# Performance work log

Measured on AMD Instinct MI355X. Metric: run time of the kernel, lower is better.

## Reference

```python
import jax, jax.numpy as jnp
import numpy as np

L, C, FC, H, W, K = 6, 256, 1024, 4, 10, 3
B, T = 4, 1024
KC = C // H


def _get_rel_emb(emb, length):
    # emb: [1, 2W+1, KC] -> [1, 2*length-1, KC]
    pad_len = max(length - (W + 1), 0)
    start = max(W + 1 - length, 0)
    if pad_len > 0:
        emb = jnp.pad(emb, ((0, 0), (pad_len, pad_len), (0, 0)))
    return emb[:, start:start + 2 * length - 1]


def _rel_to_abs(x):
    # [b,h,l,2l-1] -> [b,h,l,l] via pad/reshape shift trick
    b, h, l, _ = x.shape
    x = jnp.pad(x, ((0, 0), (0, 0), (0, 0), (0, 1)))
    x = x.reshape(b, h, l * 2 * l)
    x = jnp.pad(x, ((0, 0), (0, 0), (0, l - 1)))
    return x.reshape(b, h, l + 1, 2 * l - 1)[:, :, :l, l - 1:]


def _abs_to_rel(x):
    # [b,h,l,l] -> [b,h,l,2l-1]
    b, h, l, _ = x.shape
    x = jnp.pad(x, ((0, 0), (0, 0), (0, 0), (0, l - 1)))
    x = x.reshape(b, h, l * l + l * (l - 1))
    x = jnp.pad(x, ((0, 0), (0, 0), (l, 0)))
    return x.reshape(b, h, l, 2 * l)[:, :, :, 1:]


def _ln(x, g, b, eps=1e-5):
    # channel-wise LayerNorm over dim 1 of [B,C,T]
    m = x.mean(axis=1, keepdims=True)
    v = ((x - m) ** 2).mean(axis=1, keepdims=True)
    return (x - m) * jax.lax.rsqrt(v + eps) * g[None, :, None] + b[None, :, None]


def _conv1(x, w, b):
    # pointwise Conv1d: x [B,Cin,T], w [Cout,Cin]
    return jnp.einsum('oc,bct->bot', w, x) + b[None, :, None]


def _convk(x, w, b):
    # Conv1d: x [B,Cin,Tpad], w [Cout,Cin,K], VALID
    y = jax.lax.conv_general_dilated(x, w, (1,), 'VALID', dimension_numbers=('NCH', 'OIH', 'NCH'))
    return y + b[None, :, None]


def _attn(x, mask, wq, bq, wk, bk, wv, bv, wo, bo, erk, erv):
    b, d, t = x.shape
    q = _conv1(x, wq, bq)
    k = _conv1(x, wk, bk)
    v = _conv1(x, wv, bv)
    def split(z):
        return z.reshape(b, H, KC, t).transpose(0, 1, 3, 2)  # [b,h,t,kc]
    qh = split(q) / np.sqrt(KC).astype(np.float32)
    kh = split(k)
    vh = split(v)
    scores = jnp.einsum('bhld,bhmd->bhlm', qh, kh)
    rel_k = _get_rel_emb(erk, t)[0]  # [2t-1, kc]
    scores = scores + _rel_to_abs(jnp.einsum('bhld,md->bhlm', qh, rel_k))
    scores = jnp.where(mask == 0, jnp.float32(-1e4), scores)
    p = jax.nn.softmax(scores, axis=-1)
    out = jnp.einsum('bhlm,bhmd->bhld', p, vh)
    rel_v = _get_rel_emb(erv, t)[0]
    out = out + jnp.einsum('bhlm,md->bhld', _abs_to_rel(p), rel_v)
    out = out.transpose(0, 1, 3, 2).reshape(b, d, t)
    return _conv1(out, wo, bo)


def _ffn(x, mask, w1, b1, w2, b2):
    pl, pr = (K - 1) // 2, K // 2
    def pad_t(z):
        return jnp.pad(z * mask, ((0, 0), (0, 0), (pl, pr)))
    h = jax.nn.relu(_convk(pad_t(x), w1, b1))
    return _convk(pad_t(h), w2, b2) * mask


def setup_inputs() -> dict:
    key = jax.random.key(0)
    ks = jax.random.split(key, 12)
    s = 0.05
    return {
        'x': jax.random.normal(ks[0], (B, C, T), jnp.float32),
        'x_mask': jnp.ones((B, 1, T), jnp.float32),
        'wq': s * jax.random.normal(ks[1], (L, C, C), jnp.float32),
        'bq': jnp.zeros((L, C), jnp.float32),
        'wk': s * jax.random.normal(ks[2], (L, C, C), jnp.float32),
        'bk': jnp.zeros((L, C), jnp.float32),
        'wv': s * jax.random.normal(ks[3], (L, C, C), jnp.float32),
        'bv': jnp.zeros((L, C), jnp.float32),
        'wo': s * jax.random.normal(ks[4], (L, C, C), jnp.float32),
        'bo': jnp.zeros((L, C), jnp.float32),
        'erk': (KC ** -0.5) * jax.random.normal(ks[5], (L, 1, 2 * W + 1, KC), jnp.float32),
        'erv': (KC ** -0.5) * jax.random.normal(ks[6], (L, 1, 2 * W + 1, KC), jnp.float32),
        'ln1_g': jnp.ones((L, C), jnp.float32),
        'ln1_b': jnp.zeros((L, C), jnp.float32),
        'ffn_w1': s * jax.random.normal(ks[7], (L, FC, C, K), jnp.float32),
        'ffn_b1': jnp.zeros((L, FC), jnp.float32),
        'ffn_w2': s * jax.random.normal(ks[8], (L, C, FC, K), jnp.float32),
        'ffn_b2': jnp.zeros((L, C), jnp.float32),
        'ln2_g': jnp.ones((L, C), jnp.float32),
        'ln2_b': jnp.zeros((L, C), jnp.float32),
    }


def reference(x, x_mask, wq, bq, wk, bk, wv, bv, wo, bo, erk, erv, ln1_g, ln1_b, ffn_w1, ffn_b1, ffn_w2, ffn_b2, ln2_g, ln2_b):
    attn_mask = x_mask[:, :, None, :] * x_mask[:, :, :, None]  # [B,1,T,T]
    x = x * x_mask
    for i in range(L):
        y = _attn(x, attn_mask, wq[i], bq[i], wk[i], bk[i], wv[i], bv[i], wo[i], bo[i], erk[i], erv[i])
        x = _ln(x + y, ln1_g[i], ln1_b[i])
        y = _ffn(x, x_mask, ffn_w1[i], ffn_b1[i], ffn_w2[i], ffn_b2[i])
        x = _ln(x + y, ln2_g[i], ln2_b[i])
    return x * x_mask
```

## Files before the change

### kernel.cpp

```cpp
#include <hip/hip_runtime.h>


#define Lz 6
#define Cz 256
#define FCz 1024
#define Hz 4
#define Wz 10
#define Bz 4
#define Tz 1024
#define KCz 64
#define NR 21
#define TS 1032
#define PADF 4
#define PROWS 1026
#define MFIX 8.0f

typedef unsigned short u16;
typedef unsigned int u32;
typedef __attribute__((ext_vector_type(8))) short bf8v;
typedef __attribute__((ext_vector_type(4))) float f4v;

#define MFMA(a, b, c) __builtin_amdgcn_mfma_f32_16x16x32_bf16(a, b, c, 0, 0, 0)

__device__ inline void bf_split(float v, u16& hi, u16& lo) {
  unsigned u = __float_as_uint(v);
  unsigned hr = (u + 0x7FFFu + ((u >> 16) & 1u)) >> 16;
  float rem = v - __uint_as_float(hr << 16);
  unsigned u2 = __float_as_uint(rem);
  unsigned lr = (u2 + 0x7FFFu + ((u2 >> 16) & 1u)) >> 16;
  hi = (u16)hr;
  lo = (u16)lr;
}

__device__ inline u16 bf_rne(float v) {
  u32 u = __float_as_uint(v);
  return (u16)((u + 0x7FFFu + ((u >> 16) & 1u)) >> 16);
}

__global__ __launch_bounds__(256) void mask_in(const float* __restrict__ x,
                                               const float* __restrict__ m,
                                               float* __restrict__ xp) {
  int id = blockIdx.x * 256 + threadIdx.x;
  if (id < Bz * Cz * Tz) {
    int t = id & (Tz - 1), row = id >> 10, b = id >> 18;
    xp[(size_t)row * TS + PADF + t] = x[id] * m[b * Tz + t];
  }
}

__global__ __launch_bounds__(256) void mask_out(const float* __restrict__ xp,
                                                const float* __restrict__ m,
                                                float* __restrict__ out) {
  int id = blockIdx.x * 256 + threadIdx.x;
  if (id < Bz * Cz * Tz) {
    int t = id & (Tz - 1), row = id >> 10, b = id >> 18;
    out[id] = xp[(size_t)row * TS + PADF + t] * m[b * Tz + t];
  }
}

__global__ __launch_bounds__(256) void zero_halo(u16* hi, u16* lo, int Cd) {
  int id = blockIdx.x * 256 + threadIdx.x;
  if (id >= Bz * 2 * Cd) return;
  int c = id % Cd, rb = id / Cd, b = rb >> 1, s = rb & 1;
  size_t a = ((size_t)b * PROWS + (s ? (PROWS - 1) : 0)) * Cd + c;
  hi[a] = 0;
  lo[a] = 0;
}

__global__ __launch_bounds__(256) void tpack(const float* __restrict__ src,
                                             const float* __restrict__ mask,
                                             u16* __restrict__ dhi,
                                             u16* __restrict__ dlo, int Cd) {
  __shared__ float L[64 * 68];
  const int tid = threadIdx.x;
  const int t0 = blockIdx.x * 64, c0 = blockIdx.y * 64, b = blockIdx.z;
  const float* sb = src + (size_t)b * Cd * TS + PADF;
#pragma unroll
  for (int i = 0; i < 16; i++) {
    int id = tid + 256 * i;
    int cc = id >> 6, tt = id & 63;
    L[cc * 68 + tt] = sb[(size_t)(c0 + cc) * TS + t0 + tt];
  }
  __syncthreads();
  const int tt = tid >> 2, p = tid & 3;
  float mv = mask[(size_t)b * Tz + t0 + tt];
  u16 hs[16], ls[16];
#pragma unroll
  for (int j = 0; j < 16; j++) {
    float v = L[(p * 16 + j) * 68 + tt] * mv;
    bf_split(v, hs[j], ls[j]);
  }
  size_t da = ((size_t)b * PROWS + t0 + tt + 1) * Cd + c0 + p * 16;
  *(uint4*)&dhi[da] = *(uint4*)&hs[0];
  *(uint4*)&dhi[da + 8] = *(uint4*)&hs[8];
  *(uint4*)&dlo[da] = *(uint4*)&ls[0];
  *(uint4*)&dlo[da + 8] = *(uint4*)&ls[8];
}

__global__ __launch_bounds__(256) void pack_all(
    const float* __restrict__ wq, const float* __restrict__ wk,
    const float* __restrict__ wv, const float* __restrict__ wo_,
    const float* __restrict__ bq, const float* __restrict__ bk,
    const float* __restrict__ bv, const float* __restrict__ bo,
    const float* __restrict__ erk, const float* __restrict__ erv,
    const float* __restrict__ fw1, const float* __restrict__ fw2,
    u16* __restrict__ qwH, float* __restrict__ pb, u16* __restrict__ ekH,
    u16* __restrict__ evH, u16* __restrict__ w1H, u16* __restrict__ w1L,
    u16* __restrict__ w2H, u16* __restrict__ w2L) {
  const int blk = blockIdx.x, tid = threadIdx.x;
  if (blk < 1024) {
    int id = blk * 256 + tid;
    int o = id >> 8, c = id & 255;
    int sel = o >> 8;
    const float* w = sel == 0 ? wq : (sel == 1 ? wk : (sel == 2 ? wv : wo_));
    qwH[id] = bf_rne(w[((size_t)(o & 255) << 8) + c]);
    if (id < 1024) {
      int s2 = id >> 8;
      const float* bs = s2 == 0 ? bq : (s2 == 1 ? bk : (s2 == 2 ? bv : bo));
      pb[id] = bs[id & 255];
    }
  } else if (blk < 1040) {
    int id = (blk - 1024) * 256 + tid;
    if (id < 2048) {
      int rr = id >> 6, d = id & 63;
      ekH[id] = bf_rne((rr < NR) ? erk[rr * KCz + d] : 0.f);
    } else {
      int id2 = id - 2048;
      int d = id2 >> 5, rr = id2 & 31;
      evH[id2] = bf_rne((rr < NR) ? erv[rr * KCz + d] : 0.f);
    }
  } else if (blk < 4112) {
    int id = (blk - 1040) * 256 + tid;
    int c = id % Cz;
    int rest = id / Cz;
    int o = rest % FCz, tap = rest / FCz;
    float v = fw1[((size_t)o * Cz + c) * 3 + tap];
    bf_split(v, w1H[id], w1L[id]);
  } else {
    int id = (blk - 4112) * 256 + tid;
    int c = id % FCz;
    int rest = id / FCz;
    int o = rest % Cz, tap = rest / Cz;
    float v = fw2[((size_t)o * FCz + c) * 3 + tap];
    bf_split(v, w2H[id], w2L[id]);
  }
}

template <int EPI>
__global__ __launch_bounds__(256) void mfma_gemm2(
    const u16* __restrict__ Ah, const u16* __restrict__ Bh,
    const u16* __restrict__ Bl, const float* __restrict__ bias,
    const float* __restrict__ mask, float* __restrict__ out,
    float* __restrict__ out2, u16* __restrict__ pqh, u16* __restrict__ pql,
    u16* __restrict__ pkh, u16* __restrict__ pvh, int M, int Kc, int m_base) {
  __shared__ __align__(16) char smraw[17408];
  u16* Ash = (u16*)smraw;
  u16* Bsh = Ash + 2560;
  u16* Bsl = Bsh + 2560;
  const int tid = threadIdx.x;
  const int lane = tid & 63, wid = tid >> 6;
  const int wm = wid & 1, wn = wid >> 1;
  const int r = lane & 15, qd = lane >> 4;
  const int t0 = blockIdx.x * 64;
  const int b = blockIdx.z;
  const int srow = tid >> 2, sseg = (tid & 3) * 8;

  int m0, kc0, kcN;
  float* outp = out;
  if constexpr (EPI == 3) {
    m0 = m_base + (blockIdx.y >> 1) * 64;
    kc0 = (blockIdx.y & 1) * (Kc / 2);
    kcN = Kc / 2;
    outp = (blockIdx.y & 1) ? out2 : out;
  } else {
    m0 = blockIdx.y * 64 + m_base;
    kc0 = 0;
    kcN = Kc;
  }

  f4v acc[2][2];
#pragma unroll
  for (int i = 0; i < 2; i++)
#pragma unroll
    for (int j = 0; j < 2; j++) acc[i][j] = (f4v)(0.f);

  const size_t arow = (size_t)(m0 + srow) * Kc + kc0;
  const size_t brow = ((size_t)b * PROWS + t0 + 1 + srow) * Kc + kc0;
  for (int kc = 0; kc < kcN; kc += 32) {
    *(uint4*)&Ash[srow * 40 + sseg] = *(const uint4*)&Ah[arow + kc + sseg];
    *(uint4*)&Bsh[srow * 40 + sseg] = *(const uint4*)&Bh[brow + kc + sseg];
    *(uint4*)&Bsl[srow * 40 + sseg] = *(const uint4*)&Bl[brow + kc + sseg];
    __syncthreads();
    bf8v ah[2], bh2[2], bl2[2];
#pragma unroll
    for (int f = 0; f < 2; f++) {
      int ar = (wm * 32 + f * 16 + r) * 40 + qd * 8;
      int br = (wn * 32 + f * 16 + r) * 40 + qd * 8;
      ah[f] = *(bf8v*)&Ash[ar];
      bh2[f] = *(bf8v*)&Bsh[br];
      bl2[f] = *(bf8v*)&Bsl[br];
    }
#pragma unroll
    for (int mf = 0; mf < 2; mf++)
#pragma unroll
      for (int nf = 0; nf < 2; nf++) {
        acc[mf][nf] = MFMA(ah[mf], bh2[nf], acc[mf][nf]);
        acc[mf][nf] = MFMA(ah[mf], bl2[nf], acc[mf][nf]);
      }
    __syncthreads();
  }

  float* Ds = (float*)smraw;
  if constexpr (EPI == 0) {
    const int sel = m0 >> 8;
    const int h = (m0 >> 6) & 3;
    const int bhI = b * Hz + h;
    if (sel < 2) {
#pragma unroll
      for (int mf = 0; mf < 2; mf++)
#pragma unroll
        for (int nf = 0; nf < 2; nf++) {
          int nl = wn * 32 + nf * 16 + r;
          int ml = wm * 32 + mf * 16 + qd * 4;
          *(f4v*)&Ds[nl * 68 + ml] = acc[mf][nf];
        }
      __syncthreads();
      const int row = tid >> 2, p = tid & 3;
      size_t da = ((size_t)bhI * Tz + t0 + row) * KCz + p * 16;
      if (sel == 0) {
        u16 hs[16], ls[16];
#pragma unroll
        for (int jj = 0; jj < 4; jj++) {
          float4 dv = *(float4*)&Ds[row * 68 + p * 16 + jj * 4];
          float4 bb = *(const float4*)&bias[m0 + p * 16 + jj * 4];
          float vv[4] = {(dv.x + bb.x) * 0.125f, (dv.y + bb.y) * 0.125f,
                         (dv.z + bb.z) * 0.125f, (dv.w + bb.w) * 0.125f};
#pragma unroll
          for (int e = 0; e < 4; e++)
            bf_split(vv[e], hs[jj * 4 + e], ls[jj * 4 + e]);
        }
        *(uint4*)&pqh[da] = *(uint4*)&hs[0];
        *(uint4*)&pqh[da + 8] = *(uint4*)&hs[8];
        *(uint4*)&pql[da] = *(uint4*)&ls[0];
        *(uint4*)&pql[da + 8] = *(uint4*)&ls[8];
      } else {
        u16 hs[16];
#pragma unroll
        for (int jj = 0; jj < 4; jj++) {
          float4 dv = *(float4*)&Ds[row * 68 + p * 16 + jj * 4];
          float4 bb = *(const float4*)&bias[m0 + p * 16 + jj * 4];
          hs[jj * 4 + 0] = bf_rne(dv.x + bb.x);
          hs[jj * 4 + 1] = bf_rne(dv.y + bb.y);
          hs[jj * 4 + 2] = bf_rne(dv.z + bb.z);
          hs[jj * 4 + 3] = bf_rne(dv.w + bb.w);
        }
        *(uint4*)&pkh[da] = *(uint4*)&hs[0];
        *(uint4*)&pkh[da + 8] = *(uint4*)&hs[8];
      }
    } else {
#pragma unroll
      for (int mf = 0; mf < 2; mf++)
#pragma unroll
        for (int nf = 0; nf < 2; nf++) {
          int ml = wm * 32 + mf * 16 + qd * 4;
          int nl = wn * 32 + nf * 16 + r;
#pragma unroll
          for (int e = 0; e < 4; e++) Ds[(ml + e) * 68 + nl] = acc[mf][nf][e];
        }
      __syncthreads();
      const int row = tid >> 2, p = tid & 3;
      const float bb = bias[m0 + row];
      u16 hs[16];
#pragma unroll
      for (int jj = 0; jj < 16; jj++)
        hs[jj] = bf_rne(Ds[row * 68 + p * 16 + jj] + bb);
      size_t da = ((size_t)bhI * KCz + row) * Tz + t0 + p * 16;
      *(uint4*)&pvh[da] = *(uint4*)&hs[0];
      *(uint4*)&pvh[da + 8] = *(uint4*)&hs[8];
    }
  } else {
#pragma unroll
    for (int mf = 0; mf < 2; mf++)
#pragma unroll
      for (int nf = 0; nf < 2; nf++) {
        int ml = wm * 32 + mf * 16 + qd * 4;
        int nl = wn * 32 + nf * 16 + r;
#pragma unroll
        for (int e = 0; e < 4; e++) Ds[(ml + e) * 68 + nl] = acc[mf][nf][e];
      }
    __syncthreads();
    const int row = tid >> 2, p = tid & 3;
    size_t oa = ((size_t)b * Cz + (m0 - m_base) + row) * Tz + t0 + p * 16;
#pragma unroll
    for (int jj = 0; jj < 4; jj++)
      *(float4*)&outp[oa + jj * 4] = *(float4*)&Ds[row * 68 + p * 16 + jj * 4];
  }
}

template <int TAPS, int EPI>
__global__ __launch_bounds__(256) void mfma_gemm(
    const u16* __restrict__ Ah, const u16* __restrict__ Al,
    const u16* __restrict__ Bh, const u16* __restrict__ Bl,
    const float* __restrict__ bias, const float* __restrict__ mask,
    float* __restrict__ out, float* __restrict__ out2, u16* __restrict__ ph,
    u16* __restrict__ pl, int M, int Kc, int m_base) {
  __shared__ u16 sm[4 * 64 * 40];
  u16* Ash = sm;
  u16* Asl = sm + 2560;
  u16* Bsh = sm + 5120;
  u16* Bsl = sm + 7680;
  const int tid = threadIdx.x;
  const int lane = tid & 63, wid = tid >> 6;
  const int wm = wid & 1, wn = wid >> 1;
  const int r = lane & 15, qd = lane >> 4;
  const int t0 = blockIdx.x * 64;
  const int b = blockIdx.z;
  const int srow = tid >> 2, sseg = (tid & 3) * 8;

  int m0, kc0, kcN;
  float* outp = out;
  m0 = m_base + (blockIdx.y >> 1) * 64;
  kc0 = (blockIdx.y & 1) * (Kc / 2);
  kcN = Kc / 2;
  outp = (blockIdx.y & 1) ? out2 : out;

  f4v acc[2][2];
#pragma unroll
  for (int i = 0; i < 2; i++)
#pragma unroll
    for (int j = 0; j < 2; j++) acc[i][j] = (f4v)(0.f);

  for (int tap = 0; tap < TAPS; tap++) {
    const u16* Ath = Ah + (size_t)tap * M * Kc;
    const u16* Atl = Al + (size_t)tap * M * Kc;
    const size_t arow = (size_t)(m0 + srow) * Kc + kc0;
    const size_t brow = ((size_t)b * PROWS + t0 + tap + srow) * Kc + kc0;
    for (int kc = 0; kc < kcN; kc += 32) {
      *(uint4*)&Ash[srow * 40 + sseg] = *(const uint4*)&Ath[arow + kc + sseg];
      *(uint4*)&Asl[srow * 40 + sseg] = *(const uint4*)&Atl[arow + kc + sseg];
      *(uint4*)&Bsh[srow * 40 + sseg] = *(const uint4*)&Bh[brow + kc + sseg];
      *(uint4*)&Bsl[srow * 40 + sseg] = *(const uint4*)&Bl[brow + kc + sseg];
      __syncthreads();
      bf8v ah[2], al[2], bh[2], bl[2];
#pragma unroll
      for (int f = 0; f < 2; f++) {
        int ar = (wm * 32 + f * 16 + r) * 40 + qd * 8;
        int br = (wn * 32 + f * 16 + r) * 40 + qd * 8;
        ah[f] = *(bf8v*)&Ash[ar];
        al[f] = *(bf8v*)&Asl[ar];
        bh[f] = *(bf8v*)&Bsh[br];
        bl[f] = *(bf8v*)&Bsl[br];
      }
#pragma unroll
      for (int mf = 0; mf < 2; mf++)
#pragma unroll
        for (int nf = 0; nf < 2; nf++) {
          acc[mf][nf] = MFMA(ah[mf], bh[nf], acc[mf][nf]);
          acc[mf][nf] = MFMA(al[mf], bh[nf], acc[mf][nf]);
          acc[mf][nf] = MFMA(ah[mf], bl[nf], acc[mf][nf]);
        }
      __syncthreads();
    }
  }

  float* Ds = (float*)sm;
#pragma unroll
  for (int mf = 0; mf < 2; mf++)
#pragma unroll
    for (int nf = 0; nf < 2; nf++) {
      int ml = wm * 32 + mf * 16 + qd * 4;
      int nl = wn * 32 + nf * 16 + r;
#pragma unroll
      for (int e = 0; e < 4; e++) Ds[(ml + e) * 68 + nl] = acc[mf][nf][e];
    }
  __syncthreads();
  const int row = tid >> 2, p = tid & 3;
  size_t oa = ((size_t)b * Cz + (m0 - m_base) + row) * Tz + t0 + p * 16;
#pragma unroll
  for (int jj = 0; jj < 4; jj++)
    *(float4*)&outp[oa + jj * 4] = *(float4*)&Ds[row * 68 + p * 16 + jj * 4];
}

__global__ __launch_bounds__(256) void conv_gemm(
    const u16* __restrict__ Ah, const u16* __restrict__ Al,
    const u16* __restrict__ Bh, const u16* __restrict__ Bl,
    const float* __restrict__ bias, const float* __restrict__ mask,
    u16* __restrict__ ph, u16* __restrict__ pl, int M, int Kc) {
  __shared__ __align__(16) char smraw[34816];
  u16* Ash = (u16*)smraw;
  u16* Asl = Ash + 2560;
  u16* Bsh = Asl + 2560;
  u16* Bsl = Bsh + 5120;
  const int tid = threadIdx.x;
  const int lane = tid & 63, wid = tid >> 6;
  const int wm = wid & 1, wn = wid >> 1;
  const int r = lane & 15, qd = lane >> 4;
  const int t0 = blockIdx.x * 128;
  const int m0 = blockIdx.y * 64;
  const int b = blockIdx.z;
  const int sarow = tid >> 2, saseg = (tid & 3) * 8;
  const int sbrow = tid >> 1, sbseg = (tid & 1) * 16;

  f4v acc[2][4];
#pragma unroll
  for (int i = 0; i < 2; i++)
#pragma unroll
    for (int j = 0; j < 4; j++) acc[i][j] = (f4v)(0.f);

  for (int tap = 0; tap < 3; tap++) {
    const u16* Ath = Ah + (size_t)tap * M * Kc;
    const u16* Atl = Al + (size_t)tap * M * Kc;
    const size_t arow = (size_t)(m0 + sarow) * Kc;
    const size_t brow = ((size_t)b * PROWS + t0 + tap + sbrow) * Kc;
    for (int kc = 0; kc < Kc; kc += 32) {
      *(uint4*)&Ash[sarow * 40 + saseg] = *(const uint4*)&Ath[arow + kc + saseg];
      *(uint4*)&Asl[sarow * 40 + saseg] = *(const uint4*)&Atl[arow + kc + saseg];
      *(uint4*)&Bsh[sbrow * 40 + sbseg] = *(const uint4*)&Bh[brow + kc + sbseg];
      *(uint4*)&Bsh[sbrow * 40 + sbseg + 8] =
          *(const uint4*)&Bh[brow + kc + sbseg + 8];
      *(uint4*)&Bsl[sbrow * 40 + sbseg] = *(const uint4*)&Bl[brow + kc + sbseg];
      *(uint4*)&Bsl[sbrow * 40 + sbseg + 8] =
          *(const uint4*)&Bl[brow + kc + sbseg + 8];
      __syncthreads();
      bf8v ah[2], al[2], bh4[4], bl4[4];
#pragma unroll
      for (int mf = 0; mf < 2; mf++) {
        int ar = (wm * 32 + mf * 16 + r) * 40 + qd * 8;
        ah[mf] = *(bf8v*)&Ash[ar];
        al[mf] = *(bf8v*)&Asl[ar];
      }
#pragma unroll
      for (int nf = 0; nf < 4; nf++) {
        int br = (wn * 64 + nf * 16 + r) * 40 + qd * 8;
        bh4[nf] = *(bf8v*)&Bsh[br];
        bl4[nf] = *(bf8v*)&Bsl[br];
      }
#pragma unroll
      for (int mf = 0; mf < 2; mf++)
#pragma unroll
        for (int nf = 0; nf < 4; nf++) {
          acc[mf][nf] = MFMA(ah[mf], bh4[nf], acc[mf][nf]);
          acc[mf][nf] = MFMA(al[mf], bh4[nf], acc[mf][nf]);
          acc[mf][nf] = MFMA(ah[mf], bl4[nf], acc[mf][nf]);
        }
      __syncthreads();
    }
  }

  float* Ds = (float*)smraw;
#pragma unroll
  for (int mf = 0; mf < 2; mf++)
#pragma unroll
    for (int nf = 0; nf < 4; nf++) {
      int nl = wn * 64 + nf * 16 + r;
      int ml = wm * 32 + mf * 16 + qd * 4;
      *(f4v*)&Ds[nl * 68 + ml] = acc[mf][nf];
    }
  __syncthreads();
  const int row = tid >> 1, half = (tid & 1) * 32;
  const int t = t0 + row;
  const float mv = mask[(size_t)b * Tz + t];
  u16 hs[32], ls[32];
#pragma unroll
  for (int j = 0; j < 32; j += 4) {
    float4 dv = *(float4*)&Ds[row * 68 + half + j];
    float4 bb = *(const float4*)&bias[m0 + half + j];
    float vv[4] = {dv.x + bb.x, dv.y + bb.y, dv.z + bb.z, dv.w + bb.w};
#pragma unroll
    for (int e = 0; e < 4; e++) {
      float v = fmaxf(vv[e], 0.f) * mv;
      bf_split(v, hs[j + e], ls[j + e]);
    }
  }
  size_t da = ((size_t)b * PROWS + t + 1) * M + m0 + half;
#pragma unroll
  for (int j = 0; j < 32; j += 8) {
    *(uint4*)&ph[da + j] = *(uint4*)&hs[j];
    *(uint4*)&pl[da + j] = *(uint4*)&ls[j];
  }
}

__global__ __launch_bounds__(128, 2) void attn_mfma(
    const u16* __restrict__ Qh_, const u16* __restrict__ Ql_,
    const u16* __restrict__ Kh_, const u16* __restrict__ Vh_,
    const float* __restrict__ mask, const u16* __restrict__ erkH,
    const u16* __restrict__ ervH, float* __restrict__ O0,
    float* __restrict__ O1, float* __restrict__ O2, float* __restrict__ O3,
    float* __restrict__ lp0, float* __restrict__ lp1,
    float* __restrict__ lp2, float* __restrict__ lp3) {
  __shared__ __align__(16) char smraw[2][14336];
  const int tid = threadIdx.x;
  const int lane = tid & 63, wid = tid >> 6;
  const int r = lane & 15, qd = lane >> 4;
  const int idx = blockIdx.x;
  const int bh = idx & 15;
  const int split = (idx >> 4) & 3;
  const int i0w = (idx >> 6) * 64 + wid * 32;
  const int b = bh >> 2, h = bh & 3;
  const float* mb = mask + (size_t)b * Tz;
  const size_t qkbase = (size_t)bh * Tz * KCz;
  const size_t vbase = (size_t)bh * KCz * Tz;
  float* Op = split == 0 ? O0 : (split == 1 ? O1 : (split == 2 ? O2 : O3));
  float* lp = split == 0 ? lp0 : (split == 1 ? lp1 : (split == 2 ? lp2 : lp3));
  const int j0beg = split * 256;

  float* rqs = (float*)(smraw[wid]);
  float* bands = rqs + 704;
  u16* Pp = (u16*)(smraw[wid] + 5632);

  bf8v qh[2][2], ql[2][2];
#pragma unroll
  for (int rs = 0; rs < 2; rs++) {
    const size_t qrow = qkbase + (size_t)(i0w + rs * 16 + r) * KCz;
#pragma unroll
    for (int ks = 0; ks < 2; ks++) {
      qh[rs][ks] = *(const bf8v*)&Qh_[qrow + ks * 32 + qd * 8];
      ql[rs][ks] = *(const bf8v*)&Ql_[qrow + ks * 32 + qd * 8];
    }
  }
  for (int t = lane; t < 704; t += 64) bands[t] = -1e30f;

#pragma unroll
  for (int rs = 0; rs < 2; rs++) {
    f4v rc[2] = {(f4v)(0.f), (f4v)(0.f)};
#pragma unroll
    for (int nf = 0; nf < 2; nf++)
#pragma unroll
      for (int ks = 0; ks < 2; ks++) {
        bf8v eh = *(const bf8v*)&erkH[(16 * nf + r) * 64 + ks * 32 + qd * 8];
        rc[nf] = MFMA(qh[rs][ks], eh, rc[nf]);
        rc[nf] = MFMA(ql[rs][ks], eh, rc[nf]);
      }
#pragma unroll
    for (int nf = 0; nf < 2; nf++) {
      int rr = 16 * nf + r;
      if (rr < NR) {
#pragma unroll
        for (int e = 0; e < 4; e++)
          rqs[(rs * 16 + 4 * qd + e) * 22 + rr] = rc[nf][e];
      }
    }
  }

  float qm[2][4];
#pragma unroll
  for (int rs = 0; rs < 2; rs++)
#pragma unroll
    for (int e = 0; e < 4; e++) qm[rs][e] = mb[i0w + rs * 16 + 4 * qd + e];

  float lacc[2][4] = {};
  f4v oacc[2][4];
#pragma unroll
  for (int rs = 0; rs < 2; rs++)
#pragma unroll
    for (int nf = 0; nf < 4; nf++) oacc[rs][nf] = (f4v)(0.f);

  for (int jt = 0; jt < 4; jt++) {
    const int j0 = j0beg + jt * 64;
    bf8v kh[4][2], vh[4][2];
#pragma unroll
    for (int nf = 0; nf < 4; nf++) {
      const size_t kr = qkbase + (size_t)(j0 + 16 * nf + r) * KCz;
      const size_t vr = vbase + (size_t)(16 * nf + r) * Tz + j0;
#pragma unroll
      for (int ks = 0; ks < 2; ks++) {
        kh[nf][ks] = *(const bf8v*)&Kh_[kr + ks * 32 + qd * 8];
        vh[nf][ks] = *(const bf8v*)&Vh_[vr + ks * 32 + qd * 8];
      }
    }
    float km4[4];
#pragma unroll
    for (int nf = 0; nf < 4; nf++) km4[nf] = mb[j0 + 16 * nf + r];

#pragma unroll
    for (int rs = 0; rs < 2; rs++) {
      f4v sa[4];
#pragma unroll
      for (int nf = 0; nf < 4; nf++) sa[nf] = (f4v)(0.f);
#pragma unroll
      for (int nf = 0; nf < 4; nf++)
#pragma unroll
        for (int ks = 0; ks < 2; ks++) {
          sa[nf] = MFMA(qh[rs][ks], kh[nf][ks], sa[nf]);
          sa[nf] = MFMA(ql[rs][ks], kh[nf][ks], sa[nf]);
        }
      const int ibase = i0w + rs * 16;
      const bool diag = (j0 + 63 >= ibase - Wz) && (j0 <= ibase + 15 + Wz);
#pragma unroll
      for (int nf = 0; nf < 4; nf++)
#pragma unroll
        for (int e = 0; e < 4; e++) {
          const int iloc = rs * 16 + 4 * qd + e;
          float s = sa[nf][e];
          if (diag) {
            int dl = (j0 + 16 * nf + r) - (i0w + iloc);
            bool inb = (unsigned)(dl + Wz) <= 2u * Wz;
            if (inb) s += rqs[iloc * 22 + dl + Wz];
            if (qm[rs][e] * km4[nf] == 0.f) s = -1e4f;
            if (inb) bands[iloc * 22 + dl + Wz] = s;
          } else {
            if (qm[rs][e] * km4[nf] == 0.f) s = -1e4f;
          }
          float p = __expf(s - MFIX);
          lacc[rs][e] += p;
          Pp[iloc * 72 + 16 * nf + r] = bf_rne(p);
        }
    }
#pragma unroll
    for (int rs = 0; rs < 2; rs++)
#pragma unroll
      for (int ks = 0; ks < 2; ks++) {
        bf8v Ph = *(bf8v*)&Pp[(rs * 16 + r) * 72 + ks * 32 + qd * 8];
#pragma unroll
        for (int nf = 0; nf < 4; nf++)
          oacc[rs][nf] = MFMA(Ph, vh[nf][ks], oacc[rs][nf]);
      }
  }

  for (int t = lane; t < 32 * 32; t += 64) {
    int i = t >> 5, rr = t & 31;
    float p = (rr < NR) ? __expf(bands[i * 22 + rr] - MFIX) : 0.f;
    Pp[i * 72 + rr] = bf_rne(p);
  }
#pragma unroll
  for (int rs = 0; rs < 2; rs++) {
    bf8v Ph = *(bf8v*)&Pp[(rs * 16 + r) * 72 + qd * 8];
#pragma unroll
    for (int nf = 0; nf < 4; nf++) {
      bf8v eh = *(const bf8v*)&ervH[(16 * nf + r) * 32 + qd * 8];
      oacc[rs][nf] = MFMA(Ph, eh, oacc[rs][nf]);
    }
  }

#pragma unroll
  for (int off = 1; off < 16; off <<= 1)
#pragma unroll
    for (int rs = 0; rs < 2; rs++)
#pragma unroll
      for (int e = 0; e < 4; e++)
        lacc[rs][e] += __shfl_xor(lacc[rs][e], off, 16);
  if (r == 0) {
#pragma unroll
    for (int rs = 0; rs < 2; rs++)
#pragma unroll
      for (int e = 0; e < 4; e++)
        lp[(size_t)bh * Tz + i0w + rs * 16 + 4 * qd + e] = lacc[rs][e];
  }

  float* Os = (float*)Pp;
#pragma unroll
  for (int rs = 0; rs < 2; rs++)
#pragma unroll
    for (int nf = 0; nf < 4; nf++)
#pragma unroll
      for (int e = 0; e < 4; e++)
        Os[(rs * 16 + 4 * qd + e) * 68 + 16 * nf + r] = oacc[rs][nf][e];
#pragma unroll
  for (int rs = 0; rs < 2; rs++) {
    const float* src = &Os[(rs * 16 + r) * 68 + qd * 16];
    size_t oa = ((size_t)bh * Tz + i0w + rs * 16 + r) * KCz + qd * 16;
#pragma unroll
    for (int jj = 0; jj < 4; jj++)
      *(float4*)&Op[oa + jj * 4] = *(const float4*)&src[jj * 4];
  }
}

__global__ __launch_bounds__(256) void attn_combine(
    const float* __restrict__ O0, const float* __restrict__ O1,
    const float* __restrict__ O2, const float* __restrict__ O3,
    const float* __restrict__ l0, const float* __restrict__ l1,
    const float* __restrict__ l2, const float* __restrict__ l3,
    u16* __restrict__ outH, u16* __restrict__ outL) {
  const int bh = blockIdx.y, b = bh >> 2, h = bh & 3;
  const int i = blockIdx.x * 16 + (threadIdx.x >> 4);
  const int d0 = (threadIdx.x & 15) * 4;
  const size_t oa = ((size_t)bh * Tz + i) * KCz + d0;
  float4 a = *(const float4*)&O0[oa];
  float4 c = *(const float4*)&O1[oa];
  float4 d = *(const float4*)&O2[oa];
  float4 f = *(const float4*)&O3[oa];
  const size_t la = (size_t)bh * Tz + i;
  const float li = 1.f / (l0[la] + l1[la] + l2[la] + l3[la]);
  float v[4] = {(a.x + c.x + d.x + f.x) * li, (a.y + c.y + d.y + f.y) * li,
                (a.z + c.z + d.z + f.z) * li, (a.w + c.w + d.w + f.w) * li};
  u16 hs[4], ls[4];
#pragma unroll
  for (int e = 0; e < 4; e++) bf_split(v[e], hs[e], ls[e]);
  size_t da = ((size_t)b * PROWS + i + 1) * Cz + h * 64 + d0;
  *(uint2*)&outH[da] = *(uint2*)&hs[0];
  *(uint2*)&outL[da] = *(uint2*)&ls[0];
}

template <int VAR>
__global__ __launch_bounds__(256) void fused_ln(
    float* __restrict__ x, const float* __restrict__ y,
    const float* __restrict__ p1, const float* __restrict__ cbias,
    const float* __restrict__ g, const float* __restrict__ bb,
    const float* __restrict__ mask, u16* __restrict__ dhi,
    u16* __restrict__ dlo) {
  __shared__ float L[256 * 17];
  __shared__ float red[16][16], red2[16][16];
  __shared__ float ms[16], rs[16];
  const int tid = threadIdx.x;
  const int t0 = blockIdx.x * 16, b = blockIdx.y;
  const int tl = tid & 15, grp = tid >> 4;
  const size_t bx = (size_t)b * Cz * TS + PADF + t0 + tl;
  const size_t by = (size_t)b * Cz * Tz + t0 + tl;
  const float mv = mask[(size_t)b * Tz + t0 + tl];
  float s = 0.f, sq = 0.f;
  for (int c = grp; c < Cz; c += 16) {
    float add = y[by + (size_t)c * Tz] + p1[by + (size_t)c * Tz] + cbias[c];
    if constexpr (VAR == 1) add *= mv;
    float v = x[bx + (size_t)c * TS] + add;
    L[c * 17 + tl] = v;
    s += v;
    sq += v * v;
  }
  red[grp][tl] = s;
  red2[grp][tl] = sq;
  __syncthreads();
  if (tid < 16) {
    float su = 0.f, sqq = 0.f;
#pragma unroll
    for (int gg = 0; gg < 16; gg++) {
      su += red[gg][tid];
      sqq += red2[gg][tid];
    }
    float m = su * (1.f / Cz);
    ms[tid] = m;
    rs[tid] = rsqrtf(sqq * (1.f / Cz) - m * m + 1e-5f);
  }
  __syncthreads();
  float m = ms[tl], r = rs[tl];
  for (int c = grp; c < Cz; c += 16) {
    float v = (L[c * 17 + tl] - m) * r * g[c] + bb[c];
    x[bx + (size_t)c * TS] = v;
    L[c * 17 + tl] = v * mv;
  }
  __syncthreads();
  const int tt = tid & 15, p = tid >> 4;
  u16 hs[16], ls[16];
#pragma unroll
  for (int j = 0; j < 16; j++)
    bf_split(L[(p * 16 + j) * 17 + tt], hs[j], ls[j]);
  size_t da = ((size_t)b * PROWS + t0 + tt + 1) * Cz + p * 16;
  *(uint4*)&dhi[da] = *(uint4*)&hs[0];
  *(uint4*)&dhi[da + 8] = *(uint4*)&hs[8];
  *(uint4*)&dlo[da] = *(uint4*)&ls[0];
  *(uint4*)&dlo[da + 8] = *(uint4*)&ls[8];
}

extern "C" void kernel_launch(void* const* d_in, const int* in_sizes, int n_in,
                              void* d_out, int out_size, void* d_ws,
                              size_t ws_size, hipStream_t stream) {
  const float* x = (const float*)d_in[0];
  const float* xm = (const float*)d_in[1];
  const float* wq = (const float*)d_in[2];
  const float* bq = (const float*)d_in[3];
  const float* wk = (const float*)d_in[4];
  const float* bk = (const float*)d_in[5];
  const float* wv = (const float*)d_in[6];
  const float* bv = (const float*)d_in[7];
  const float* wo = (const float*)d_in[8];
  const float* bo = (const float*)d_in[9];
  const float* erk = (const float*)d_in[10];
  const float* erv = (const float*)d_in[11];
  const float* g1 = (const float*)d_in[12];
  const float* b1 = (const float*)d_in[13];
  const float* fw1 = (const float*)d_in[14];
  const float* fb1 = (const float*)d_in[15];
  const float* fw2 = (const float*)d_in[16];
  const float* fb2 = (const float*)d_in[17];
  const float* g2 = (const float*)d_in[18];
  const float* b2 = (const float*)d_in[19];

  const size_t NBC = (size_t)Bz * Cz * Tz;
  const size_t XBN = (size_t)Bz * Cz * TS;
  const size_t HP = (size_t)Bz * PROWS * FCz;
  const size_t XP = (size_t)Bz * PROWS * Cz;
  const size_t QS = (size_t)Bz * Hz * Tz * KCz;

  float* ws = (float*)d_ws;
  float* xb = ws;
  float* yb = xb + XBN;
  float* p1 = yb + NBC;
  float* unf = p1 + NBC;
  u16* hpH = (u16*)unf;
  u16* hpL = hpH + HP;
  u16* Qh = (u16*)unf;
  u16* Ql = Qh + QS;
  u16* Kh = Ql + QS;
  u16* Vh = Kh + QS;
  float* O2buf = (float*)(Vh + QS);
  float* xpf = unf + HP;
  u16* xpH = (u16*)xpf;
  u16* xpL = xpH + XP;
  float* qwf = xpf + XP;
  u16* qwH = (u16*)qwf;
  float* w1f = qwf + 131072;
  u16* w1H = (u16*)w1f;
  u16* w1L = w1H + 786432;
  float* w2f = w1f + 786432;
  u16* w2H = (u16*)w2f;
  u16* w2L = w2H + 786432;
  float* erf = w2f + 786432;
  u16* ekH = (u16*)erf;
  u16* evH = ekH + 2048;
  float* pbias = erf + 2048;
  float* lb0 = pbias + 1024;
  float* lb1 = lb0 + 16384;
  float* lb2 = lb1 + 16384;
  float* lb3 = lb2 + 16384;
  float* O3buf = lb3 + 16384;

  const int ntot = (int)NBC;
  mask_in<<<dim3((ntot + 255) / 256), 256, 0, stream>>>(x, xm, xb);
  zero_halo<<<dim3((Bz * 2 * Cz + 255) / 256), 256, 0, stream>>>(xpH, xpL, Cz);
  tpack<<<dim3(16, 4, 4), 256, 0, stream>>>(xb, xm, xpH, xpL, Cz);

  for (int l = 0; l < Lz; l++) {
    pack_all<<<dim3(7184), 256, 0, stream>>>(
        wq + (size_t)l * Cz * Cz, wk + (size_t)l * Cz * Cz,
        wv + (size_t)l * Cz * Cz, wo + (size_t)l * Cz * Cz, bq + l * Cz,
        bk + l * Cz, bv + l * Cz, bo + l * Cz, erk + (size_t)l * NR * KCz,
        erv + (size_t)l * NR * KCz, fw1 + (size_t)l * FCz * Cz * 3,
        fw2 + (size_t)l * Cz * FCz * 3, qwH, pbias, ekH, evH, w1H, w1L, w2H,
        w2L);
    mfma_gemm2<0><<<dim3(16, 12, 4), 256, 0, stream>>>(
        qwH, xpH, xpL, pbias, xm, nullptr, nullptr, Qh, Ql, Kh, Vh, 1024, Cz,
        0);
    attn_mfma<<<dim3(1024), 128, 0, stream>>>(Qh, Ql, Kh, Vh, xm, ekH, evH,
                                              yb, p1, O2buf, O3buf, lb0, lb1,
                                              lb2, lb3);
    attn_combine<<<dim3(64, 16), 256, 0, stream>>>(yb, p1, O2buf, O3buf, lb0,
                                                   lb1, lb2, lb3, xpH, xpL);
    mfma_gemm2<3><<<dim3(16, 8, 4), 256, 0, stream>>>(
        qwH, xpH, xpL, pbias, xm, yb, p1, nullptr, nullptr, nullptr, nullptr,
        1024, Cz, 768);
    fused_ln<2><<<dim3(64, 4), 256, 0, stream>>>(
        xb, yb, p1, bo + l * Cz, g1 + l * Cz, b1 + l * Cz, xm, xpH, xpL);
    zero_halo<<<dim3((Bz * 2 * FCz + 255) / 256), 256, 0, stream>>>(hpH, hpL,
                                                                    FCz);
    conv_gemm<<<dim3(8, 16, 4), 256, 0, stream>>>(
        w1H, w1L, xpH, xpL, fb1 + l * FCz, xm, hpH, hpL, FCz, Cz);
    mfma_gemm<3, 3><<<dim3(16, 8, 4), 256, 0, stream>>>(
        w2H, w2L, hpH, hpL, nullptr, xm, yb, p1, nullptr, nullptr, Cz, FCz, 0);
    fused_ln<1><<<dim3(64, 4), 256, 0, stream>>>(
        xb, yb, p1, fb2 + l * Cz, g2 + l * Cz, b2 + l * Cz, xm, xpH, xpL);
  }
  mask_out<<<dim3((ntot + 255) / 256), 256, 0, stream>>>(xb, xm,
                                                         (float*)d_out);
}
```

Before: 1.069 ms.

## Pack all layer weights once, drop low weight split, reuse conv kernel for FFN2

```diff
diff --git a/kernel.cpp b/kernel.cpp
--- a/kernel.cpp
+++ b/kernel.cpp
@@ -103,45 +103,56 @@
     const float* __restrict__ bv, const float* __restrict__ bo,
     const float* __restrict__ erk, const float* __restrict__ erv,
     const float* __restrict__ fw1, const float* __restrict__ fw2,
-    u16* __restrict__ qwH, float* __restrict__ pb, u16* __restrict__ ekH,
-    u16* __restrict__ evH, u16* __restrict__ w1H, u16* __restrict__ w1L,
-    u16* __restrict__ w2H, u16* __restrict__ w2L) {
+    u16* __restrict__ qwAll, float* __restrict__ pbAll,
+    u16* __restrict__ ekAll, u16* __restrict__ evAll,
+    u16* __restrict__ w1All, u16* __restrict__ w2All) {
   const int blk = blockIdx.x, tid = threadIdx.x;
-  if (blk < 1024) {
-    int id = blk * 256 + tid;
+  const int layer = blk / 7184;
+  const int bl = blk % 7184;
+  if (bl < 1024) {
+    int id = bl * 256 + tid;
     int o = id >> 8, c = id & 255;
     int sel = o >> 8;
-    const float* w = sel == 0 ? wq : (sel == 1 ? wk : (sel == 2 ? wv : wo_));
-    qwH[id] = bf_rne(w[((size_t)(o & 255) << 8) + c]);
+    const size_t wof = (size_t)layer * Cz * Cz;
+    const float* w = sel == 0 ? wq + wof
+                              : (sel == 1 ? wk + wof
+                                          : (sel == 2 ? wv + wof : wo_ + wof));
+    qwAll[(size_t)layer * 262144 + id] = bf_rne(w[((o & 255) << 8) + c]);
     if (id < 1024) {
       int s2 = id >> 8;
       const float* bs = s2 == 0 ? bq : (s2 == 1 ? bk : (s2 == 2 ? bv : bo));
-      pb[id] = bs[id & 255];
-    }
-  } else if (blk < 1040) {
-    int id = (blk - 1024) * 256 + tid;
+      pbAll[layer * 1024 + id] = bs[layer * Cz + (id & 255)];
+    }
+  } else if (bl < 1040) {
+    int id = (bl - 1024) * 256 + tid;
     if (id < 2048) {
       int rr = id >> 6, d = id & 63;
-      ekH[id] = bf_rne((rr < NR) ? erk[rr * KCz + d] : 0.f);
+      ekAll[layer * 2048 + id] =
+          bf_rne((rr < NR) ? erk[(size_t)layer * NR * KCz + rr * KCz + d]
+                           : 0.f);
     } else {
       int id2 = id - 2048;
       int d = id2 >> 5, rr = id2 & 31;
-      evH[id2] = bf_rne((rr < NR) ? erv[rr * KCz + d] : 0.f);
-    }
-  } else if (blk < 4112) {
-    int id = (blk - 1040) * 256 + tid;
+      evAll[layer * 2048 + id2] =
+          bf_rne((rr < NR) ? erv[(size_t)layer * NR * KCz + rr * KCz + d]
+                           : 0.f);
+    }
+  } else if (bl < 4112) {
+    int id = (bl - 1040) * 256 + tid;
     int c = id % Cz;
     int rest = id / Cz;
     int o = rest % FCz, tap = rest / FCz;
-    float v = fw1[((size_t)o * Cz + c) * 3 + tap];
-    bf_split(v, w1H[id], w1L[id]);
+    w1All[(size_t)layer * 786432 + id] =
+        bf_rne(fw1[(size_t)layer * FCz * Cz * 3 + ((size_t)o * Cz + c) * 3 +
+                   tap]);
   } else {
-    int id = (blk - 4112) * 256 + tid;
+    int id = (bl - 4112) * 256 + tid;
     int c = id % FCz;
     int rest = id / FCz;
     int o = rest % Cz, tap = rest / Cz;
-    float v = fw2[((size_t)o * FCz + c) * 3 + tap];
-    bf_split(v, w2H[id], w2L[id]);
+    w2All[(size_t)layer * 786432 + id] =
+        bf_rne(fw2[(size_t)layer * Cz * FCz * 3 + ((size_t)o * FCz + c) * 3 +
+                   tap]);
   }
 }
 
@@ -296,110 +307,40 @@
   }
 }
 
-template <int TAPS, int EPI>
-__global__ __launch_bounds__(256) void mfma_gemm(
-    const u16* __restrict__ Ah, const u16* __restrict__ Al,
-    const u16* __restrict__ Bh, const u16* __restrict__ Bl,
-    const float* __restrict__ bias, const float* __restrict__ mask,
-    float* __restrict__ out, float* __restrict__ out2, u16* __restrict__ ph,
-    u16* __restrict__ pl, int M, int Kc, int m_base) {
-  __shared__ u16 sm[4 * 64 * 40];
-  u16* Ash = sm;
-  u16* Asl = sm + 2560;
-  u16* Bsh = sm + 5120;
-  u16* Bsl = sm + 7680;
-  const int tid = threadIdx.x;
-  const int lane = tid & 63, wid = tid >> 6;
-  const int wm = wid & 1, wn = wid >> 1;
-  const int r = lane & 15, qd = lane >> 4;
-  const int t0 = blockIdx.x * 64;
-  const int b = blockIdx.z;
-  const int srow = tid >> 2, sseg = (tid & 3) * 8;
-
-  int m0, kc0, kcN;
-  float* outp = out;
-  m0 = m_base + (blockIdx.y >> 1) * 64;
-  kc0 = (blockIdx.y & 1) * (Kc / 2);
-  kcN = Kc / 2;
-  outp = (blockIdx.y & 1) ? out2 : out;
-
-  f4v acc[2][2];
-#pragma unroll
-  for (int i = 0; i < 2; i++)
-#pragma unroll
-    for (int j = 0; j < 2; j++) acc[i][j] = (f4v)(0.f);
-
-  for (int tap = 0; tap < TAPS; tap++) {
-    const u16* Ath = Ah + (size_t)tap * M * Kc;
-    const u16* Atl = Al + (size_t)tap * M * Kc;
-    const size_t arow = (size_t)(m0 + srow) * Kc + kc0;
-    const size_t brow = ((size_t)b * PROWS + t0 + tap + srow) * Kc + kc0;
-    for (int kc = 0; kc < kcN; kc += 32) {
-      *(uint4*)&Ash[srow * 40 + sseg] = *(const uint4*)&Ath[arow + kc + sseg];
-      *(uint4*)&Asl[srow * 40 + sseg] = *(const uint4*)&Atl[arow + kc + sseg];
-      *(uint4*)&Bsh[srow * 40 + sseg] = *(const uint4*)&Bh[brow + kc + sseg];
-      *(uint4*)&Bsl[srow * 40 + sseg] = *(const uint4*)&Bl[brow + kc + sseg];
-      __syncthreads();
-      bf8v ah[2], al[2], bh[2], bl[2];
-#pragma unroll
-      for (int f = 0; f < 2; f++) {
-        int ar = (wm * 32 + f * 16 + r) * 40 + qd * 8;
-        int br = (wn * 32 + f * 16 + r) * 40 + qd * 8;
-        ah[f] = *(bf8v*)&Ash[ar];
-        al[f] = *(bf8v*)&Asl[ar];
-        bh[f] = *(bf8v*)&Bsh[br];
-        bl[f] = *(bf8v*)&Bsl[br];
-      }
-#pragma unroll
-      for (int mf = 0; mf < 2; mf++)
-#pragma unroll
-        for (int nf = 0; nf < 2; nf++) {
-          acc[mf][nf] = MFMA(ah[mf], bh[nf], acc[mf][nf]);
-          acc[mf][nf] = MFMA(al[mf], bh[nf], acc[mf][nf]);
-          acc[mf][nf] = MFMA(ah[mf], bl[nf], acc[mf][nf]);
-        }
-      __syncthreads();
-    }
-  }
-
-  float* Ds = (float*)sm;
-#pragma unroll
-  for (int mf = 0; mf < 2; mf++)
-#pragma unroll
-    for (int nf = 0; nf < 2; nf++) {
-      int ml = wm * 32 + mf * 16 + qd * 4;
-      int nl = wn * 32 + nf * 16 + r;
-#pragma unroll
-      for (int e = 0; e < 4; e++) Ds[(ml + e) * 68 + nl] = acc[mf][nf][e];
-    }
-  __syncthreads();
-  const int row = tid >> 2, p = tid & 3;
-  size_t oa = ((size_t)b * Cz + (m0 - m_base) + row) * Tz + t0 + p * 16;
-#pragma unroll
-  for (int jj = 0; jj < 4; jj++)
-    *(float4*)&outp[oa + jj * 4] = *(float4*)&Ds[row * 68 + p * 16 + jj * 4];
-}
-
-__global__ __launch_bounds__(256) void conv_gemm(
-    const u16* __restrict__ Ah, const u16* __restrict__ Al,
-    const u16* __restrict__ Bh, const u16* __restrict__ Bl,
-    const float* __restrict__ bias, const float* __restrict__ mask,
-    u16* __restrict__ ph, u16* __restrict__ pl, int M, int Kc) {
+template <int EPI>
+__global__ __launch_bounds__(256) void conv_mfma(
+    const u16* __restrict__ Ah, const u16* __restrict__ Bh,
+    const u16* __restrict__ Bl, const float* __restrict__ bias,
+    const float* __restrict__ mask, u16* __restrict__ ph,
+    u16* __restrict__ pl, float* __restrict__ o0, float* __restrict__ o1,
+    float* __restrict__ o2, float* __restrict__ o3, int M, int Kc) {
   __shared__ __align__(16) char smraw[34816];
   u16* Ash = (u16*)smraw;
-  u16* Asl = Ash + 2560;
-  u16* Bsh = Asl + 2560;
+  u16* Bsh = Ash + 2560;
   u16* Bsl = Bsh + 5120;
   const int tid = threadIdx.x;
   const int lane = tid & 63, wid = tid >> 6;
   const int wm = wid & 1, wn = wid >> 1;
   const int r = lane & 15, qd = lane >> 4;
   const int t0 = blockIdx.x * 128;
-  const int m0 = blockIdx.y * 64;
   const int b = blockIdx.z;
   const int sarow = tid >> 2, saseg = (tid & 3) * 8;
   const int sbrow = tid >> 1, sbseg = (tid & 1) * 16;
 
+  int m0, kc0, kcN;
+  float* outp = nullptr;
+  if constexpr (EPI == 3) {
+    int mt = blockIdx.y >> 2, sp = blockIdx.y & 3;
+    m0 = mt * 64;
+    kc0 = sp * (Kc / 4);
+    kcN = Kc / 4;
+    outp = sp == 0 ? o0 : (sp == 1 ? o1 : (sp == 2 ? o2 : o3));
+  } else {
+    m0 = blockIdx.y * 64;
+    kc0 = 0;
+    kcN = Kc;
+  }
+
   f4v acc[2][4];
 #pragma unroll
   for (int i = 0; i < 2; i++)
@@ -407,13 +348,11 @@
     for (int j = 0; j < 4; j++) acc[i][j] = (f4v)(0.f);
 
   for (int tap = 0; tap < 3; tap++) {
-    const u16* Ath = Ah + (size_t)tap * M * Kc;
-    const u16* Atl = Al + (size_t)tap * M * Kc;
-    const size_t arow = (size_t)(m0 + sarow) * Kc;
-    const size_t brow = ((size_t)b * PROWS + t0 + tap + sbrow) * Kc;
-    for (int kc = 0; kc < Kc; kc += 32) {
-      *(uint4*)&Ash[sarow * 40 + saseg] = *(const uint4*)&Ath[arow + kc + saseg];
-      *(uint4*)&Asl[sarow * 40 + saseg] = *(const uint4*)&Atl[arow + kc + saseg];
+    const u16* At = Ah + (size_t)tap * M * Kc;
+    const size_t arow = (size_t)(m0 + sarow) * Kc + kc0;
+    const size_t brow = ((size_t)b * PROWS + t0 + tap + sbrow) * Kc + kc0;
+    for (int kc = 0; kc < kcN; kc += 32) {
+      *(uint4*)&Ash[sarow * 40 + saseg] = *(const uint4*)&At[arow + kc + saseg];
       *(uint4*)&Bsh[sbrow * 40 + sbseg] = *(const uint4*)&Bh[brow + kc + sbseg];
       *(uint4*)&Bsh[sbrow * 40 + sbseg + 8] =
           *(const uint4*)&Bh[brow + kc + sbseg + 8];
@@ -421,13 +360,10 @@
       *(uint4*)&Bsl[sbrow * 40 + sbseg + 8] =
           *(const uint4*)&Bl[brow + kc + sbseg + 8];
       __syncthreads();
-      bf8v ah[2], al[2], bh4[4], bl4[4];
-#pragma unroll
-      for (int mf = 0; mf < 2; mf++) {
-        int ar = (wm * 32 + mf * 16 + r) * 40 + qd * 8;
-        ah[mf] = *(bf8v*)&Ash[ar];
-        al[mf] = *(bf8v*)&Asl[ar];
-      }
+      bf8v ah[2], bh4[4], bl4[4];
+#pragma unroll
+      for (int mf = 0; mf < 2; mf++)
+        ah[mf] = *(bf8v*)&Ash[(wm * 32 + mf * 16 + r) * 40 + qd * 8];
 #pragma unroll
       for (int nf = 0; nf < 4; nf++) {
         int br = (wn * 64 + nf * 16 + r) * 40 + qd * 8;
@@ -439,43 +375,61 @@
 #pragma unroll
         for (int nf = 0; nf < 4; nf++) {
           acc[mf][nf] = MFMA(ah[mf], bh4[nf], acc[mf][nf]);
-          acc[mf][nf] = MFMA(al[mf], bh4[nf], acc[mf][nf]);
           acc[mf][nf] = MFMA(ah[mf], bl4[nf], acc[mf][nf]);
         }
       __syncthreads();
     }
   }
 
-  float* Ds = (float*)smraw;
-#pragma unroll
-  for (int mf = 0; mf < 2; mf++)
-#pragma unroll
-    for (int nf = 0; nf < 4; nf++) {
-      int nl = wn * 64 + nf * 16 + r;
-      int ml = wm * 32 + mf * 16 + qd * 4;
-      *(f4v*)&Ds[nl * 68 + ml] = acc[mf][nf];
-    }
-  __syncthreads();
-  const int row = tid >> 1, half = (tid & 1) * 32;
-  const int t = t0 + row;
-  const float mv = mask[(size_t)b * Tz + t];
-  u16 hs[32], ls[32];
-#pragma unroll
-  for (int j = 0; j < 32; j += 4) {
-    float4 dv = *(float4*)&Ds[row * 68 + half + j];
-    float4 bb = *(const float4*)&bias[m0 + half + j];
-    float vv[4] = {dv.x + bb.x, dv.y + bb.y, dv.z + bb.z, dv.w + bb.w};
-#pragma unroll
-    for (int e = 0; e < 4; e++) {
-      float v = fmaxf(vv[e], 0.f) * mv;
-      bf_split(v, hs[j + e], ls[j + e]);
-    }
-  }
-  size_t da = ((size_t)b * PROWS + t + 1) * M + m0 + half;
-#pragma unroll
-  for (int j = 0; j < 32; j += 8) {
-    *(uint4*)&ph[da + j] = *(uint4*)&hs[j];
-    *(uint4*)&pl[da + j] = *(uint4*)&ls[j];
+  if constexpr (EPI == 1) {
+    float* Ds = (float*)smraw;
+#pragma unroll
+    for (int mf = 0; mf < 2; mf++)
+#pragma unroll
+      for (int nf = 0; nf < 4; nf++) {
+        int nl = wn * 64 + nf * 16 + r;
+        int ml = wm * 32 + mf * 16 + qd * 4;
+        *(f4v*)&Ds[nl * 68 + ml] = acc[mf][nf];
+      }
+    __syncthreads();
+    const int row = tid >> 1, half = (tid & 1) * 32;
+    const int t = t0 + row;
+    const float mv = mask[(size_t)b * Tz + t];
+    u16 hs[32], ls[32];
+#pragma unroll
+    for (int j = 0; j < 32; j += 4) {
+      float4 dv = *(float4*)&Ds[row * 68 + half + j];
+      float4 bb = *(const float4*)&bias[m0 + half + j];
+      float vv[4] = {dv.x + bb.x, dv.y + bb.y, dv.z + bb.z, dv.w + bb.w};
+#pragma unroll
+      for (int e = 0; e < 4; e++) {
+        float v = fmaxf(vv[e], 0.f) * mv;
+        bf_split(v, hs[j + e], ls[j + e]);
+      }
+    }
+    size_t da = ((size_t)b * PROWS + t + 1) * M + m0 + half;
+#pragma unroll
+    for (int j = 0; j < 32; j += 8) {
+      *(uint4*)&ph[da + j] = *(uint4*)&hs[j];
+      *(uint4*)&pl[da + j] = *(uint4*)&ls[j];
+    }
+  } else {
+    float* Ds = (float*)smraw;
+#pragma unroll
+    for (int mf = 0; mf < 2; mf++)
+#pragma unroll
+      for (int nf = 0; nf < 4; nf++) {
+        int ml = wm * 32 + mf * 16 + qd * 4;
+        int nl = wn * 64 + nf * 16 + r;
+#pragma unroll
+        for (int e = 0; e < 4; e++) Ds[(ml + e) * 132 + nl] = acc[mf][nf][e];
+      }
+    __syncthreads();
+    const int row = tid >> 2, seg = (tid & 3) * 32;
+    size_t oa = ((size_t)b * Cz + m0 + row) * Tz + t0 + seg;
+#pragma unroll
+    for (int j = 0; j < 8; j++)
+      *(float4*)&outp[oa + j * 4] = *(float4*)&Ds[row * 132 + seg + j * 4];
   }
 }
 
@@ -554,6 +508,7 @@
 #pragma unroll
     for (int nf = 0; nf < 4; nf++) oacc[rs][nf] = (f4v)(0.f);
 
+#pragma unroll 2
   for (int jt = 0; jt < 4; jt++) {
     const int j0 = j0beg + jt * 64;
     bf8v kh[4][2], vh[4][2];
@@ -690,10 +645,11 @@
   *(uint2*)&outL[da] = *(uint2*)&ls[0];
 }
 
-template <int VAR>
+template <int VAR, int NP>
 __global__ __launch_bounds__(256) void fused_ln(
     float* __restrict__ x, const float* __restrict__ y,
-    const float* __restrict__ p1, const float* __restrict__ cbias,
+    const float* __restrict__ p1, const float* __restrict__ p2,
+    const float* __restrict__ p3, const float* __restrict__ cbias,
     const float* __restrict__ g, const float* __restrict__ bb,
     const float* __restrict__ mask, u16* __restrict__ dhi,
     u16* __restrict__ dlo) {
@@ -709,6 +665,8 @@
   float s = 0.f, sq = 0.f;
   for (int c = grp; c < Cz; c += 16) {
     float add = y[by + (size_t)c * Tz] + p1[by + (size_t)c * Tz] + cbias[c];
+    if constexpr (NP == 4)
+      add += p2[by + (size_t)c * Tz] + p3[by + (size_t)c * Tz];
     if constexpr (VAR == 1) add *= mv;
     float v = x[bx + (size_t)c * TS] + add;
     L[c * 17 + tl] = v;
@@ -783,69 +741,67 @@
   float* xb = ws;
   float* yb = xb + XBN;
   float* p1 = yb + NBC;
-  float* unf = p1 + NBC;
+  float* p2 = p1 + NBC;
+  float* p3 = p2 + NBC;
+  float* unf = p3 + NBC;
   u16* hpH = (u16*)unf;
   u16* hpL = hpH + HP;
   u16* Qh = (u16*)unf;
   u16* Ql = Qh + QS;
   u16* Kh = Ql + QS;
   u16* Vh = Kh + QS;
-  float* O2buf = (float*)(Vh + QS);
   float* xpf = unf + HP;
   u16* xpH = (u16*)xpf;
   u16* xpL = xpH + XP;
   float* qwf = xpf + XP;
-  u16* qwH = (u16*)qwf;
-  float* w1f = qwf + 131072;
-  u16* w1H = (u16*)w1f;
-  u16* w1L = w1H + 786432;
-  float* w2f = w1f + 786432;
-  u16* w2H = (u16*)w2f;
-  u16* w2L = w2H + 786432;
-  float* erf = w2f + 786432;
-  u16* ekH = (u16*)erf;
-  u16* evH = ekH + 2048;
-  float* pbias = erf + 2048;
-  float* lb0 = pbias + 1024;
+  u16* qwAll = (u16*)qwf;
+  float* w1f = qwf + 786432;
+  u16* w1All = (u16*)w1f;
+  float* w2f = w1f + 2359296;
+  u16* w2All = (u16*)w2f;
+  float* erf = w2f + 2359296;
+  u16* ekAll = (u16*)erf;
+  u16* evAll = ekAll + 12288;
+  float* pbAll = erf + 12288;
+  float* lb0 = pbAll + 6144;
   float* lb1 = lb0 + 16384;
   float* lb2 = lb1 + 16384;
   float* lb3 = lb2 + 16384;
-  float* O3buf = lb3 + 16384;
 
   const int ntot = (int)NBC;
+  pack_all<<<dim3(6 * 7184), 256, 0, stream>>>(
+      wq, wk, wv, wo, bq, bk, bv, bo, erk, erv, fw1, fw2, qwAll, pbAll, ekAll,
+      evAll, w1All, w2All);
   mask_in<<<dim3((ntot + 255) / 256), 256, 0, stream>>>(x, xm, xb);
   zero_halo<<<dim3((Bz * 2 * Cz + 255) / 256), 256, 0, stream>>>(xpH, xpL, Cz);
   tpack<<<dim3(16, 4, 4), 256, 0, stream>>>(xb, xm, xpH, xpL, Cz);
 
   for (int l = 0; l < Lz; l++) {
-    pack_all<<<dim3(7184), 256, 0, stream>>>(
-        wq + (size_t)l * Cz * Cz, wk + (size_t)l * Cz * Cz,
-        wv + (size_t)l * Cz * Cz, wo + (size_t)l * Cz * Cz, bq + l * Cz,
-        bk + l * Cz, bv + l * Cz, bo + l * Cz, erk + (size_t)l * NR * KCz,
-        erv + (size_t)l * NR * KCz, fw1 + (size_t)l * FCz * Cz * 3,
-        fw2 + (size_t)l * Cz * FCz * 3, qwH, pbias, ekH, evH, w1H, w1L, w2H,
-        w2L);
     mfma_gemm2<0><<<dim3(16, 12, 4), 256, 0, stream>>>(
-        qwH, xpH, xpL, pbias, xm, nullptr, nullptr, Qh, Ql, Kh, Vh, 1024, Cz,
-        0);
-    attn_mfma<<<dim3(1024), 128, 0, stream>>>(Qh, Ql, Kh, Vh, xm, ekH, evH,
-                                              yb, p1, O2buf, O3buf, lb0, lb1,
-                                              lb2, lb3);
-    attn_combine<<<dim3(64, 16), 256, 0, stream>>>(yb, p1, O2buf, O3buf, lb0,
-                                                   lb1, lb2, lb3, xpH, xpL);
+        qwAll + (size_t)l * 262144, xpH, xpL, pbAll + l * 1024, xm, nullptr,
+        nullptr, Qh, Ql, Kh, Vh, 1024, Cz, 0);
+    attn_mfma<<<dim3(1024), 128, 0, stream>>>(
+        Qh, Ql, Kh, Vh, xm, ekAll + l * 2048, evAll + l * 2048, yb, p1, p2, p3,
+        lb0, lb1, lb2, lb3);
+    attn_combine<<<dim3(64, 16), 256, 0, stream>>>(yb, p1, p2, p3, lb0, lb1,
+                                                   lb2, lb3, xpH, xpL);
     mfma_gemm2<3><<<dim3(16, 8, 4), 256, 0, stream>>>(
-        qwH, xpH, xpL, pbias, xm, yb, p1, nullptr, nullptr, nullptr, nullptr,
-        1024, Cz, 768);
-    fused_ln<2><<<dim3(64, 4), 256, 0, stream>>>(
-        xb, yb, p1, bo + l * Cz, g1 + l * Cz, b1 + l * Cz, xm, xpH, xpL);
+        qwAll + (size_t)l * 262144, xpH, xpL, pbAll + l * 1024, xm, yb, p1,
+        nullptr, nullptr, nullptr, nullptr, 1024, Cz, 768);
+    fused_ln<2, 2><<<dim3(64, 4), 256, 0, stream>>>(
+        xb, yb, p1, nullptr, nullptr, bo + l * Cz, g1 + l * Cz, b1 + l * Cz,
+        xm, xpH, xpL);
     zero_halo<<<dim3((Bz * 2 * FCz + 255) / 256), 256, 0, stream>>>(hpH, hpL,
                                                                     FCz);
-    conv_gemm<<<dim3(8, 16, 4), 256, 0, stream>>>(
-        w1H, w1L, xpH, xpL, fb1 + l * FCz, xm, hpH, hpL, FCz, Cz);
-    mfma_gemm<3, 3><<<dim3(16, 8, 4), 256, 0, stream>>>(
-        w2H, w2L, hpH, hpL, nullptr, xm, yb, p1, nullptr, nullptr, Cz, FCz, 0);
-    fused_ln<1><<<dim3(64, 4), 256, 0, stream>>>(
-        xb, yb, p1, fb2 + l * Cz, g2 + l * Cz, b2 + l * Cz, xm, xpH, xpL);
+    conv_mfma<1><<<dim3(8, 16, 4), 256, 0, stream>>>(
+        w1All + (size_t)l * 786432, xpH, xpL, fb1 + l * FCz, xm, hpH, hpL,
+        nullptr, nullptr, nullptr, nullptr, FCz, Cz);
+    conv_mfma<3><<<dim3(8, 16, 4), 256, 0, stream>>>(
+        w2All + (size_t)l * 786432, hpH, hpL, nullptr, xm, nullptr, nullptr,
+        yb, p1, p2, p3, Cz, FCz);
+    fused_ln<1, 4><<<dim3(64, 4), 256, 0, stream>>>(
+        xb, yb, p1, p2, p3, fb2 + l * Cz, g2 + l * Cz, b2 + l * Cz, xm, xpH,
+        xpL);
   }
   mask_out<<<dim3((ntot + 255) / 256), 256, 0, stream>>>(xb, xm,
                                                          (float*)d_out);
```

Measured after the change: 1.002 ms. -6.3%, faster.
